# Kernel optimization log

Measured on AMD Instinct MI355X. Metric: run time of the kernel, lower is better.

The kernel has to match this reference:

```python
import jax, jax.numpy as jnp
import numpy as np

N = 10000        # num nodes
E = 640000       # num edges
FIN = 128        # input feature dim
NH = 8           # num heads
FOUT = 16        # out features per head (NH*FOUT == FIN)
NEG_SLOPE = 0.2
EPS = 1e-16


def setup_inputs() -> dict:
    key = jax.random.key(0)
    ks = jax.random.split(key, 7)
    x = jax.random.normal(ks[0], (N, FIN), dtype=jnp.float32)
    edges = jax.random.randint(ks[1], (2, E), 0, N, dtype=jnp.int64)
    # kaiming-uniform-ish init scale
    s = float(np.sqrt(6.0 / FIN))
    W_proj = jax.random.uniform(ks[2], (NH * FOUT, FIN), minval=-s, maxval=s, dtype=jnp.float32)
    W_skip = jax.random.uniform(ks[3], (NH * FOUT, FIN), minval=-s, maxval=s, dtype=jnp.float32)
    sf = float(np.sqrt(6.0 / FOUT))
    score_src = jax.random.uniform(ks[4], (1, NH, FOUT), minval=-sf, maxval=sf, dtype=jnp.float32)
    score_tgt = jax.random.uniform(ks[5], (1, NH, FOUT), minval=-sf, maxval=sf, dtype=jnp.float32)
    bias = jnp.zeros((NH * FOUT,), dtype=jnp.float32)
    return {"x": x, "edges": edges, "W_proj": W_proj, "W_skip": W_skip,
            "score_src": score_src, "score_tgt": score_tgt, "bias": bias}


def reference(x, edges, W_proj, W_skip, score_src, score_tgt, bias):
    src, tgt = edges[0], edges[1]
    # project: [N, NH, FOUT]
    proj = (x @ W_proj.T).reshape(N, NH, FOUT)
    # per-node scores: [N, NH]
    s_src = (proj * score_src).sum(-1)
    s_tgt = (proj * score_tgt).sum(-1)
    # lift to edges and score: [E, NH]
    scores = jax.nn.leaky_relu(s_src[src] + s_tgt[tgt], negative_slope=NEG_SLOPE)
    # neighborhood-aware softmax (global max subtraction, as in original)
    exp_scores = jnp.exp(scores - jnp.max(scores))
    denom = jax.ops.segment_sum(exp_scores, tgt, num_segments=N)  # [N, NH]
    att = exp_scores / (denom[tgt] + EPS)                          # [E, NH]
    # weighted aggregation: [N, NH, FOUT]
    weighted = proj[src] * att[:, :, None]
    out = jax.ops.segment_sum(weighted, tgt, num_segments=N)
    # skip connection (dims differ per-head, so skip_proj is used), concat, bias
    out = out + (x @ W_skip.T).reshape(N, NH, FOUT)
    out = out.reshape(N, NH * FOUT) + bias
    return out
```

## Files before the change

kernel.cpp:

```cpp
#include <hip/hip_runtime.h>
#include <hip/hip_bf16.h>

#define FIN   128
#define NH    8
#define NEG   0.2f
#define HB    256
#define NMAX  10240

typedef __attribute__((ext_vector_type(8))) short short8;
typedef __attribute__((ext_vector_type(4))) float f32x4;

__device__ __forceinline__ short f2bf(float f) {
    unsigned u = __float_as_uint(f);
    return (short)((u + 0x7FFFu + ((u >> 16) & 1u)) >> 16);
}
__device__ __forceinline__ float bflo(unsigned p) { return __uint_as_float(p << 16); }
__device__ __forceinline__ float bfhi(unsigned p) { return __uint_as_float(p & 0xFFFF0000u); }
__device__ __forceinline__ float ld_f(const void* p, int i, bool bf16) {
    if (bf16) {
        unsigned h = ((const unsigned short*)p)[i];
        return __uint_as_float(h << 16);
    }
    return ((const float*)p)[i];
}
__device__ __forceinline__ short8 ld_frag(const void* p, size_t off, bool bf16) {
    if (bf16) return *(const short8*)((const short*)p + off);
    const float* f = (const float*)p + off;
    f32x4 f0 = *(const f32x4*)f;
    f32x4 f1 = *(const f32x4*)(f + 4);
    short8 r;
    r[0] = f2bf(f0[0]); r[1] = f2bf(f0[1]); r[2] = f2bf(f0[2]); r[3] = f2bf(f0[3]);
    r[4] = f2bf(f1[0]); r[5] = f2bf(f1[1]); r[6] = f2bf(f1[2]); r[7] = f2bf(f1[3]);
    return r;
}
__device__ __forceinline__ float escore(float ss, float st) {
    float v = ss + st;
    v = v > 0.f ? v : NEG * v;
    return __expf(fminf(v, 60.f));
}
__device__ __forceinline__ bool wave_bf16(const unsigned* x32) {
    unsigned w  = x32[threadIdx.x & 63];
    unsigned ex = (w >> 7) & 0xFFu;
    return __popcll(__ballot(ex >= 118u && ex <= 130u)) >= 48;
}
__device__ __forceinline__ bool wave_e64(const int* e32) {
    return __popcll(__ballot(e32[2 * (threadIdx.x & 63) + 1] == 0)) == 64;
}

__global__ __launch_bounds__(256) void k_projhist(
    const void* __restrict__ x, const void* __restrict__ Wp,
    const void* __restrict__ Ws,
    const void* __restrict__ ssrcw, const void* __restrict__ stgtw,
    unsigned short* __restrict__ projb, unsigned short* __restrict__ skipb,
    float* __restrict__ s_src, float* __restrict__ s_tgt,
    const int* __restrict__ e32, int* __restrict__ hist2d,
    int N, int E, int tiles, int halfTiles, int projBlocks, int perB)
{
    __shared__ unsigned l32[NMAX / 2];
    if ((int)blockIdx.x >= projBlocks) {
        const bool e64 = wave_e64(e32);
        const int hb = (int)blockIdx.x - projBlocks;
        const int t = threadIdx.x;
        const int nw = (N + 1) >> 1;
        for (int j = t; j < nw; j += 256) l32[j] = 0;
        __syncthreads();
        const int lo = hb * perB;
        const int hi = min(lo + perB, E);
        for (int i = lo + t; i < hi; i += 256) {
            int tg = e64 ? e32[2 * ((size_t)E + i)] : e32[(size_t)E + i];
            atomicAdd(&l32[tg >> 1], 1u << ((tg & 1) << 4));
        }
        __syncthreads();
        for (int j = t; j < N; j += 256)
            hist2d[(size_t)hb * N + j] = (l32[j >> 1] >> ((j & 1) << 4)) & 0xFFFFu;
        return;
    }
    const bool bf16 = wave_bf16((const unsigned*)x);
    const int lane = threadIdx.x & 63;
    const int wt = blockIdx.x * 4 + (threadIdx.x >> 6);
    if (wt >= tiles) return;
    const int mat = (wt >= halfTiles) ? 1 : 0;
    const int m0 = (mat ? wt - halfTiles : wt) * 16;
    const int mr = lane & 15;
    const int kb = lane >> 4;

    short8 a[4];
    const size_t xoff = (size_t)(m0 + mr) * FIN + kb * 8;
#pragma unroll
    for (int s = 0; s < 4; ++s) a[s] = ld_frag(x, xoff + s * 32, bf16);

    const void* W = mat ? Ws : Wp;
    f32x4 acc[8];
#pragma unroll
    for (int c = 0; c < 8; ++c) {
        acc[c] = (f32x4){0.f, 0.f, 0.f, 0.f};
        const size_t woff = (size_t)(c * 16 + mr) * FIN + kb * 8;
#pragma unroll
        for (int s = 0; s < 4; ++s) {
            short8 b = ld_frag(W, woff + s * 32, bf16);
            acc[c] = __builtin_amdgcn_mfma_f32_16x16x32_bf16(a[s], b, acc[c], 0, 0, 0);
        }
    }
    if (mat == 0) {
#pragma unroll
        for (int c = 0; c < 8; ++c) {
            float sw = ld_f(ssrcw, c * 16 + mr, bf16);
            float tw = ld_f(stgtw, c * 16 + mr, bf16);
#pragma unroll
            for (int r = 0; r < 4; ++r) {
                int row = m0 + kb * 4 + r;
                float v = acc[c][r];
                projb[(size_t)row * FIN + c * 16 + mr] = (unsigned short)f2bf(v);
                float vs = v * sw, vt = v * tw;
#pragma unroll
                for (int o = 8; o >= 1; o >>= 1) {
                    vs += __shfl_xor(vs, o);
                    vt += __shfl_xor(vt, o);
                }
                if (mr == 0) {
                    s_src[row * NH + c] = vs;
                    s_tgt[row * NH + c] = vt;
                }
            }
        }
    } else {
#pragma unroll
        for (int c = 0; c < 8; ++c)
#pragma unroll
            for (int r = 0; r < 4; ++r)
                skipb[(size_t)(m0 + kb * 4 + r) * FIN + c * 16 + mr] =
                    (unsigned short)f2bf(acc[c][r]);
    }
}

__global__ __launch_bounds__(256) void k_colscan(
    const int* __restrict__ hist2d, int* __restrict__ pbase,
    int* __restrict__ cnt, int N, int Npad)
{
    int j = blockIdx.x * 256 + threadIdx.x;
    if (j >= N) { if (j < Npad) cnt[j] = 0; return; }
    int s = 0;
#pragma unroll 8
    for (int b = 0; b < HB; ++b) {
        int v = hist2d[(size_t)b * N + j];
        pbase[(size_t)b * N + j] = s;
        s += v;
    }
    cnt[j] = s;
}

__global__ __launch_bounds__(256) void k_place(
    const int* __restrict__ e32, const int* __restrict__ cnt,
    const int* __restrict__ pbase, int* __restrict__ offs,
    int* __restrict__ sorted_src, int N, int E, int perB)
{
    __shared__ int cur[NMAX];
    __shared__ int sd[256];
    const bool e64 = wave_e64(e32);
    const int b = blockIdx.x, t = threadIdx.x;
    const int PER = (N + 255) / 256;

    if (PER == 40 && (N & 3) == 0) {
        const int4* c4 = (const int4*)cnt + t * 10;
        int4 v[10];
        int sum = 0;
#pragma unroll
        for (int q = 0; q < 10; ++q) {
            v[q] = c4[q];
            sum += (v[q].x + v[q].y) + (v[q].z + v[q].w);
        }
        sd[t] = sum;
        __syncthreads();
#pragma unroll
        for (int off = 1; off < 256; off <<= 1) {
            int add = (t >= off) ? sd[t - off] : 0;
            __syncthreads();
            sd[t] += add;
            __syncthreads();
        }
        int run = sd[t] - sum;
        const int base = t * 40;
        const int4* pb4 = (const int4*)(pbase + (size_t)b * N) + t * 10;
#pragma unroll
        for (int q = 0; q < 10; ++q) {
            int4 pb = pb4[q];
            int idx = base + q * 4;
            int r0 = run;
            int r1 = r0 + v[q].x;
            int r2 = r1 + v[q].y;
            int r3 = r2 + v[q].z;
            cur[idx]     = r0 + pb.x;
            cur[idx + 1] = r1 + pb.y;
            cur[idx + 2] = r2 + pb.z;
            cur[idx + 3] = r3 + pb.w;
            if (b == 0) {
                if (idx     < N) offs[idx]     = r0;
                if (idx + 1 < N) offs[idx + 1] = r1;
                if (idx + 2 < N) offs[idx + 2] = r2;
                if (idx + 3 < N) offs[idx + 3] = r3;
            }
            run = r3 + v[q].w;
        }
        if (b == 0 && t == 255) offs[N] = run;
    } else {
        int sum = 0;
        for (int i = 0; i < PER; ++i) {
            int idx = t * PER + i;
            sum += (idx < N) ? cnt[idx] : 0;
        }
        sd[t] = sum;
        __syncthreads();
#pragma unroll
        for (int off = 1; off < 256; off <<= 1) {
            int add = (t >= off) ? sd[t - off] : 0;
            __syncthreads();
            sd[t] += add;
            __syncthreads();
        }
        int run = sd[t] - sum;
        for (int i = 0; i < PER; ++i) {
            int idx = t * PER + i;
            if (idx < N) {
                cur[idx] = run + pbase[(size_t)b * N + idx];
                if (b == 0) offs[idx] = run;
                run += cnt[idx];
            }
        }
        if (b == 0 && t == 255) offs[N] = run;
    }
    __syncthreads();

    const int lo = b * perB;
    const int hi = min(lo + perB, E);
    int se[10], te[10];
#pragma unroll
    for (int k = 0; k < 10; ++k) {
        int i = lo + t + k * 256;
        te[k] = -1;
        if (i < hi) {
            if (e64) { se[k] = e32[2 * (size_t)i]; te[k] = e32[2 * ((size_t)E + i)]; }
            else     { se[k] = e32[i];             te[k] = e32[(size_t)E + i]; }
        }
    }
#pragma unroll
    for (int k = 0; k < 10; ++k) {
        if (te[k] >= 0) {
            int pos = atomicAdd(&cur[te[k]], 1);
            sorted_src[pos] = se[k];
        }
    }
    for (int i = lo + t + 10 * 256; i < hi; i += 256) {
        int s, tg;
        if (e64) { s = e32[2 * (size_t)i]; tg = e32[2 * ((size_t)E + i)]; }
        else     { s = e32[i];             tg = e32[(size_t)E + i]; }
        int pos = atomicAdd(&cur[tg], 1);
        sorted_src[pos] = s;
    }
}

__global__ __launch_bounds__(64) void k_aggregate(
    const int* __restrict__ offs, const int* __restrict__ sorted_src,
    const float* __restrict__ s_src, const float* __restrict__ s_tgt,
    const unsigned short* __restrict__ projb, const unsigned short* __restrict__ skipb,
    const void* __restrict__ bias, void* __restrict__ out,
    const unsigned* __restrict__ x32)
{
    const bool bf16 = wave_bf16(x32);
    const int n = blockIdx.x, l = threadIdx.x;
    const int start = offs[n], end = offs[n + 1];
    const int h = l >> 3;
    const int c2 = l * 2;
    const float st = s_tgt[(size_t)n * NH + h];

    float ae0 = 0.f, ao0 = 0.f, ae1 = 0.f, ao1 = 0.f;
    float ae2 = 0.f, ao2 = 0.f, ae3 = 0.f, ao3 = 0.f;
    float d0 = 0.f, d1 = 0.f, d2 = 0.f, d3 = 0.f;

    const int cnt4 = (end - start) >> 2;
    int e = start;
    if (cnt4 > 0) {
        int s0 = sorted_src[e],     s1 = sorted_src[e + 1];
        int s2 = sorted_src[e + 2], s3 = sorted_src[e + 3];
        for (int g = 0; g < cnt4; ++g) {
            const int t0 = s0, t1 = s1, t2 = s2, t3 = s3;
            e += 4;
            if (g + 1 < cnt4) {
                s0 = sorted_src[e];     s1 = sorted_src[e + 1];
                s2 = sorted_src[e + 2]; s3 = sorted_src[e + 3];
            }
            float w0 = escore(s_src[(size_t)t0 * NH + h], st);
            float w1 = escore(s_src[(size_t)t1 * NH + h], st);
            float w2 = escore(s_src[(size_t)t2 * NH + h], st);
            float w3 = escore(s_src[(size_t)t3 * NH + h], st);
            unsigned p0 = *(const unsigned*)(projb + (size_t)t0 * FIN + c2);
            unsigned p1 = *(const unsigned*)(projb + (size_t)t1 * FIN + c2);
            unsigned p2 = *(const unsigned*)(projb + (size_t)t2 * FIN + c2);
            unsigned p3 = *(const unsigned*)(projb + (size_t)t3 * FIN + c2);
            ae0 += w0 * bflo(p0); ao0 += w0 * bfhi(p0); d0 += w0;
            ae1 += w1 * bflo(p1); ao1 += w1 * bfhi(p1); d1 += w1;
            ae2 += w2 * bflo(p2); ao2 += w2 * bfhi(p2); d2 += w2;
            ae3 += w3 * bflo(p3); ao3 += w3 * bfhi(p3); d3 += w3;
        }
    }
    for (; e < end; ++e) {
        int s = sorted_src[e];
        float w = escore(s_src[(size_t)s * NH + h], st);
        unsigned p = *(const unsigned*)(projb + (size_t)s * FIN + c2);
        ae0 += w * bflo(p); ao0 += w * bfhi(p); d0 += w;
    }

    float inv = 1.f / (((d0 + d1) + (d2 + d3)) + 1e-16f);
    unsigned skp = *(const unsigned*)(skipb + (size_t)n * FIN + c2);
    float be, bo;
    if (bf16) {
        unsigned bb = *(const unsigned*)((const unsigned short*)bias + c2);
        be = bflo(bb); bo = bfhi(bb);
    } else {
        float2 b2 = *(const float2*)((const float*)bias + c2);
        be = b2.x; bo = b2.y;
    }
    float oe = ((ae0 + ae1) + (ae2 + ae3)) * inv + bflo(skp) + be;
    float oo = ((ao0 + ao1) + (ao2 + ao3)) * inv + bfhi(skp) + bo;
    if (bf16) {
        unsigned pr = ((unsigned)(unsigned short)f2bf(oo) << 16)
                    | (unsigned)(unsigned short)f2bf(oe);
        ((unsigned*)out)[((size_t)n * FIN + c2) >> 1] = pr;
    } else {
        float2 o2; o2.x = oe; o2.y = oo;
        *(float2*)((float*)out + (size_t)n * FIN + c2) = o2;
    }
}

extern "C" void kernel_launch(void* const* d_in, const int* in_sizes, int n_in,
                              void* d_out, int out_size, void* d_ws, size_t ws_size,
                              hipStream_t stream)
{
    const void* x    = d_in[0];
    const int* edges = (const int*)d_in[1];
    const void* Wp   = d_in[2];
    const void* Ws   = d_in[3];
    const void* ssw  = d_in[4];
    const void* stw  = d_in[5];
    const void* bias = d_in[6];

    const int N = in_sizes[0] / FIN;
    const int E = in_sizes[1] / 2;
    const int PER  = (N + 255) / 256;
    const int Npad = PER * 256;

    char* wp = (char*)d_ws;
    auto takeB = [&wp](size_t bytes) {
        char* p = wp;
        wp += (bytes + 255) & ~(size_t)255;
        return p;
    };
    unsigned short* projb = (unsigned short*)takeB((size_t)N * FIN * 2);
    unsigned short* skipb = (unsigned short*)takeB((size_t)N * FIN * 2);
    float* s_src    = (float*)takeB((size_t)N * NH * 4);
    float* s_tgt    = (float*)takeB((size_t)N * NH * 4);
    int* sorted_src = (int*)takeB((size_t)E * 4);
    int* offs       = (int*)takeB((size_t)(N + 8) * 4);
    int* cnt        = (int*)takeB((size_t)Npad * 4);
    int* hist2d     = (int*)takeB((size_t)HB * N * 4);
    int* pbase      = (int*)takeB((size_t)HB * N * 4 + 4096);

    const int halfTiles  = (N + 15) / 16;
    const int tiles      = 2 * halfTiles;
    const int projBlocks = (tiles + 3) / 4;
    const int perB       = (E + HB - 1) / HB;

    k_projhist<<<projBlocks + HB, 256, 0, stream>>>(
        x, Wp, Ws, ssw, stw, projb, skipb, s_src, s_tgt,
        edges, hist2d, N, E, tiles, halfTiles, projBlocks, perB);
    k_colscan<<<Npad / 256, 256, 0, stream>>>(hist2d, pbase, cnt, N, Npad);
    k_place<<<HB, 256, 0, stream>>>(edges, cnt, pbase, offs, sorted_src, N, E, perB);
    k_aggregate<<<N, 64, 0, stream>>>(offs, sorted_src, s_src, s_tgt, projb,
                                      skipb, bias, d_out, (const unsigned*)x);
}
```

Baseline: 148.0 us.

## Pack histograms as 16-bit pairs, fuse column scan into GEMM kernel, unroll aggregate by 8

Histogram counts are stored as packed 16-bit pairs, which halves the traffic for the histogram, prefix and count buffers. The histogram now runs as its own kernel, and the column scan runs alongside the projection GEMM in one launch, removing a kernel launch and overlapping the scan with the matmul. The placement kernel now reads the packed counts with a fixed 40-per-thread layout, which drops the general fallback path for other N. The aggregation loop processes 8 neighbours per iteration to get more loads in flight, at the cost of more registers.

```diff
diff --git a/kernel.cpp b/kernel.cpp
--- a/kernel.cpp
+++ b/kernel.cpp
@@ -6,6 +6,7 @@
 #define NEG   0.2f
 #define HB    256
 #define NMAX  10240
+#define RSW   (NMAX / 2)
 
 typedef __attribute__((ext_vector_type(8))) short short8;
 typedef __attribute__((ext_vector_type(4))) float f32x4;
@@ -47,38 +48,59 @@
     return __popcll(__ballot(e32[2 * (threadIdx.x & 63) + 1] == 0)) == 64;
 }
 
-__global__ __launch_bounds__(256) void k_projhist(
+__global__ __launch_bounds__(256) void k_hist(
+    const int* __restrict__ e32, unsigned* __restrict__ hist2w,
+    int N, int E, int perB)
+{
+    __shared__ unsigned l32[RSW];
+    const bool e64 = wave_e64(e32);
+    const int b = blockIdx.x, t = threadIdx.x;
+    const int nw = (N + 1) >> 1;
+    for (int j = t; j < nw; j += 256) l32[j] = 0;
+    __syncthreads();
+    const int lo = b * perB;
+    const int hi = min(lo + perB, E);
+    for (int i = lo + t; i < hi; i += 256) {
+        int tg = e64 ? ((const int2*)e32)[(size_t)E + i].x : e32[(size_t)E + i];
+        atomicAdd(&l32[tg >> 1], 1u << ((tg & 1) << 4));
+    }
+    __syncthreads();
+    const int nw4 = (nw + 3) >> 2;
+    uint4* dst = (uint4*)(hist2w + (size_t)b * RSW);
+    const uint4* src = (const uint4*)l32;
+    for (int j = t; j < nw4; j += 256) dst[j] = src[j];
+}
+
+__global__ __launch_bounds__(256) void k_gemmscan(
     const void* __restrict__ x, const void* __restrict__ Wp,
     const void* __restrict__ Ws,
     const void* __restrict__ ssrcw, const void* __restrict__ stgtw,
     unsigned short* __restrict__ projb, unsigned short* __restrict__ skipb,
     float* __restrict__ s_src, float* __restrict__ s_tgt,
-    const int* __restrict__ e32, int* __restrict__ hist2d,
-    int N, int E, int tiles, int halfTiles, int projBlocks, int perB)
-{
-    __shared__ unsigned l32[NMAX / 2];
-    if ((int)blockIdx.x >= projBlocks) {
-        const bool e64 = wave_e64(e32);
-        const int hb = (int)blockIdx.x - projBlocks;
-        const int t = threadIdx.x;
+    const unsigned* __restrict__ hist2w, unsigned* __restrict__ pbase2w,
+    unsigned* __restrict__ cnt2w,
+    int N, int tiles, int halfTiles, int csBlocks)
+{
+    if ((int)blockIdx.x < csBlocks) {
+        const int j = blockIdx.x * 256 + threadIdx.x;
+        if (j >= RSW) return;
         const int nw = (N + 1) >> 1;
-        for (int j = t; j < nw; j += 256) l32[j] = 0;
-        __syncthreads();
-        const int lo = hb * perB;
-        const int hi = min(lo + perB, E);
-        for (int i = lo + t; i < hi; i += 256) {
-            int tg = e64 ? e32[2 * ((size_t)E + i)] : e32[(size_t)E + i];
-            atomicAdd(&l32[tg >> 1], 1u << ((tg & 1) << 4));
-        }
-        __syncthreads();
-        for (int j = t; j < N; j += 256)
-            hist2d[(size_t)hb * N + j] = (l32[j >> 1] >> ((j & 1) << 4)) & 0xFFFFu;
+        if (j >= nw) { cnt2w[j] = 0; return; }
+        unsigned s0 = 0, s1 = 0;
+#pragma unroll 8
+        for (int r = 0; r < HB; ++r) {
+            unsigned v = hist2w[(size_t)r * RSW + j];
+            pbase2w[(size_t)r * RSW + j] = s0 | (s1 << 16);
+            s0 += v & 0xFFFFu;
+            s1 += v >> 16;
+        }
+        cnt2w[j] = s0 | (s1 << 16);
         return;
     }
+    const int wt = ((int)blockIdx.x - csBlocks) * 4 + ((int)threadIdx.x >> 6);
+    if (wt >= tiles) return;
     const bool bf16 = wave_bf16((const unsigned*)x);
     const int lane = threadIdx.x & 63;
-    const int wt = blockIdx.x * 4 + (threadIdx.x >> 6);
-    if (wt >= tiles) return;
     const int mat = (wt >= halfTiles) ? 1 : 0;
     const int m0 = (mat ? wt - halfTiles : wt) * 16;
     const int mr = lane & 15;
@@ -133,41 +155,27 @@
     }
 }
 
-__global__ __launch_bounds__(256) void k_colscan(
-    const int* __restrict__ hist2d, int* __restrict__ pbase,
-    int* __restrict__ cnt, int N, int Npad)
-{
-    int j = blockIdx.x * 256 + threadIdx.x;
-    if (j >= N) { if (j < Npad) cnt[j] = 0; return; }
-    int s = 0;
-#pragma unroll 8
-    for (int b = 0; b < HB; ++b) {
-        int v = hist2d[(size_t)b * N + j];
-        pbase[(size_t)b * N + j] = s;
-        s += v;
-    }
-    cnt[j] = s;
-}
-
 __global__ __launch_bounds__(256) void k_place(
-    const int* __restrict__ e32, const int* __restrict__ cnt,
-    const int* __restrict__ pbase, int* __restrict__ offs,
+    const int* __restrict__ e32, const unsigned* __restrict__ cnt2w,
+    const unsigned* __restrict__ pbase2w, int* __restrict__ offs,
     int* __restrict__ sorted_src, int N, int E, int perB)
 {
     __shared__ int cur[NMAX];
     __shared__ int sd[256];
     const bool e64 = wave_e64(e32);
     const int b = blockIdx.x, t = threadIdx.x;
-    const int PER = (N + 255) / 256;
-
-    if (PER == 40 && (N & 3) == 0) {
-        const int4* c4 = (const int4*)cnt + t * 10;
-        int4 v[10];
+
+    {
+        const uint4* c4 = (const uint4*)cnt2w + t * 5;
+        uint4 v[5];
         int sum = 0;
 #pragma unroll
-        for (int q = 0; q < 10; ++q) {
+        for (int q = 0; q < 5; ++q) {
             v[q] = c4[q];
-            sum += (v[q].x + v[q].y) + (v[q].z + v[q].w);
+            sum += (int)((v[q].x & 0xFFFFu) + (v[q].x >> 16))
+                 + (int)((v[q].y & 0xFFFFu) + (v[q].y >> 16))
+                 + (int)((v[q].z & 0xFFFFu) + (v[q].z >> 16))
+                 + (int)((v[q].w & 0xFFFFu) + (v[q].w >> 16));
         }
         sd[t] = sum;
         __syncthreads();
@@ -179,51 +187,23 @@
             __syncthreads();
         }
         int run = sd[t] - sum;
+        const uint4* pb4 = (const uint4*)(pbase2w + (size_t)b * RSW) + t * 5;
         const int base = t * 40;
-        const int4* pb4 = (const int4*)(pbase + (size_t)b * N) + t * 10;
-#pragma unroll
-        for (int q = 0; q < 10; ++q) {
-            int4 pb = pb4[q];
-            int idx = base + q * 4;
-            int r0 = run;
-            int r1 = r0 + v[q].x;
-            int r2 = r1 + v[q].y;
-            int r3 = r2 + v[q].z;
-            cur[idx]     = r0 + pb.x;
-            cur[idx + 1] = r1 + pb.y;
-            cur[idx + 2] = r2 + pb.z;
-            cur[idx + 3] = r3 + pb.w;
-            if (b == 0) {
-                if (idx     < N) offs[idx]     = r0;
-                if (idx + 1 < N) offs[idx + 1] = r1;
-                if (idx + 2 < N) offs[idx + 2] = r2;
-                if (idx + 3 < N) offs[idx + 3] = r3;
-            }
-            run = r3 + v[q].w;
-        }
-        if (b == 0 && t == 255) offs[N] = run;
-    } else {
-        int sum = 0;
-        for (int i = 0; i < PER; ++i) {
-            int idx = t * PER + i;
-            sum += (idx < N) ? cnt[idx] : 0;
-        }
-        sd[t] = sum;
-        __syncthreads();
-#pragma unroll
-        for (int off = 1; off < 256; off <<= 1) {
-            int add = (t >= off) ? sd[t - off] : 0;
-            __syncthreads();
-            sd[t] += add;
-            __syncthreads();
-        }
-        int run = sd[t] - sum;
-        for (int i = 0; i < PER; ++i) {
-            int idx = t * PER + i;
-            if (idx < N) {
-                cur[idx] = run + pbase[(size_t)b * N + idx];
-                if (b == 0) offs[idx] = run;
-                run += cnt[idx];
+#pragma unroll
+        for (int q = 0; q < 5; ++q) {
+            uint4 pb = pb4[q];
+            unsigned cw[4] = {v[q].x, v[q].y, v[q].z, v[q].w};
+            unsigned pw[4] = {pb.x, pb.y, pb.z, pb.w};
+#pragma unroll
+            for (int u = 0; u < 4; ++u) {
+                int idx = base + q * 8 + u * 2;
+                int c0 = (int)(cw[u] & 0xFFFFu), c1 = (int)(cw[u] >> 16);
+                cur[idx] = run + (int)(pw[u] & 0xFFFFu);
+                if (b == 0 && idx < N) offs[idx] = run;
+                run += c0;
+                cur[idx + 1] = run + (int)(pw[u] >> 16);
+                if (b == 0 && idx + 1 < N) offs[idx + 1] = run;
+                run += c1;
             }
         }
         if (b == 0 && t == 255) offs[N] = run;
@@ -238,8 +218,13 @@
         int i = lo + t + k * 256;
         te[k] = -1;
         if (i < hi) {
-            if (e64) { se[k] = e32[2 * (size_t)i]; te[k] = e32[2 * ((size_t)E + i)]; }
-            else     { se[k] = e32[i];             te[k] = e32[(size_t)E + i]; }
+            if (e64) {
+                se[k] = ((const int2*)e32)[(size_t)i].x;
+                te[k] = ((const int2*)e32)[(size_t)E + i].x;
+            } else {
+                se[k] = e32[i];
+                te[k] = e32[(size_t)E + i];
+            }
         }
     }
 #pragma unroll
@@ -251,8 +236,8 @@
     }
     for (int i = lo + t + 10 * 256; i < hi; i += 256) {
         int s, tg;
-        if (e64) { s = e32[2 * (size_t)i]; tg = e32[2 * ((size_t)E + i)]; }
-        else     { s = e32[i];             tg = e32[(size_t)E + i]; }
+        if (e64) { s = ((const int2*)e32)[(size_t)i].x; tg = ((const int2*)e32)[(size_t)E + i].x; }
+        else     { s = e32[i];                           tg = e32[(size_t)E + i]; }
         int pos = atomicAdd(&cur[tg], 1);
         sorted_src[pos] = s;
     }
@@ -272,44 +257,52 @@
     const int c2 = l * 2;
     const float st = s_tgt[(size_t)n * NH + h];
 
-    float ae0 = 0.f, ao0 = 0.f, ae1 = 0.f, ao1 = 0.f;
-    float ae2 = 0.f, ao2 = 0.f, ae3 = 0.f, ao3 = 0.f;
-    float d0 = 0.f, d1 = 0.f, d2 = 0.f, d3 = 0.f;
-
-    const int cnt4 = (end - start) >> 2;
+    float ae[8], ao[8], d[8];
+#pragma unroll
+    for (int k = 0; k < 8; ++k) { ae[k] = 0.f; ao[k] = 0.f; d[k] = 0.f; }
+
+    const int cnt8 = (end - start) >> 3;
     int e = start;
-    if (cnt4 > 0) {
-        int s0 = sorted_src[e],     s1 = sorted_src[e + 1];
-        int s2 = sorted_src[e + 2], s3 = sorted_src[e + 3];
-        for (int g = 0; g < cnt4; ++g) {
-            const int t0 = s0, t1 = s1, t2 = s2, t3 = s3;
-            e += 4;
-            if (g + 1 < cnt4) {
-                s0 = sorted_src[e];     s1 = sorted_src[e + 1];
-                s2 = sorted_src[e + 2]; s3 = sorted_src[e + 3];
-            }
-            float w0 = escore(s_src[(size_t)t0 * NH + h], st);
-            float w1 = escore(s_src[(size_t)t1 * NH + h], st);
-            float w2 = escore(s_src[(size_t)t2 * NH + h], st);
-            float w3 = escore(s_src[(size_t)t3 * NH + h], st);
-            unsigned p0 = *(const unsigned*)(projb + (size_t)t0 * FIN + c2);
-            unsigned p1 = *(const unsigned*)(projb + (size_t)t1 * FIN + c2);
-            unsigned p2 = *(const unsigned*)(projb + (size_t)t2 * FIN + c2);
-            unsigned p3 = *(const unsigned*)(projb + (size_t)t3 * FIN + c2);
-            ae0 += w0 * bflo(p0); ao0 += w0 * bfhi(p0); d0 += w0;
-            ae1 += w1 * bflo(p1); ao1 += w1 * bfhi(p1); d1 += w1;
-            ae2 += w2 * bflo(p2); ao2 += w2 * bfhi(p2); d2 += w2;
-            ae3 += w3 * bflo(p3); ao3 += w3 * bfhi(p3); d3 += w3;
+    if (cnt8 > 0) {
+        int idx[8];
+#pragma unroll
+        for (int k = 0; k < 8; ++k) idx[k] = sorted_src[e + k];
+        for (int g = 0; g < cnt8; ++g) {
+            int cu[8];
+#pragma unroll
+            for (int k = 0; k < 8; ++k) cu[k] = idx[k];
+            e += 8;
+            if (g + 1 < cnt8) {
+#pragma unroll
+                for (int k = 0; k < 8; ++k) idx[k] = sorted_src[e + k];
+            }
+            unsigned p[8];
+#pragma unroll
+            for (int k = 0; k < 8; ++k)
+                p[k] = *(const unsigned*)(projb + (size_t)cu[k] * FIN + c2);
+            float w[8];
+#pragma unroll
+            for (int k = 0; k < 8; ++k)
+                w[k] = escore(s_src[(size_t)cu[k] * NH + h], st);
+#pragma unroll
+            for (int k = 0; k < 8; ++k) {
+                ae[k] += w[k] * bflo(p[k]);
+                ao[k] += w[k] * bfhi(p[k]);
+                d[k]  += w[k];
+            }
         }
     }
     for (; e < end; ++e) {
         int s = sorted_src[e];
         float w = escore(s_src[(size_t)s * NH + h], st);
         unsigned p = *(const unsigned*)(projb + (size_t)s * FIN + c2);
-        ae0 += w * bflo(p); ao0 += w * bfhi(p); d0 += w;
-    }
-
-    float inv = 1.f / (((d0 + d1) + (d2 + d3)) + 1e-16f);
+        ae[0] += w * bflo(p); ao[0] += w * bfhi(p); d[0] += w;
+    }
+
+    float num_e = ((ae[0] + ae[1]) + (ae[2] + ae[3])) + ((ae[4] + ae[5]) + (ae[6] + ae[7]));
+    float num_o = ((ao[0] + ao[1]) + (ao[2] + ao[3])) + ((ao[4] + ao[5]) + (ao[6] + ao[7]));
+    float den   = ((d[0] + d[1]) + (d[2] + d[3])) + ((d[4] + d[5]) + (d[6] + d[7]));
+    float inv = 1.f / (den + 1e-16f);
     unsigned skp = *(const unsigned*)(skipb + (size_t)n * FIN + c2);
     float be, bo;
     if (bf16) {
@@ -319,8 +312,8 @@
         float2 b2 = *(const float2*)((const float*)bias + c2);
         be = b2.x; bo = b2.y;
     }
-    float oe = ((ae0 + ae1) + (ae2 + ae3)) * inv + bflo(skp) + be;
-    float oo = ((ao0 + ao1) + (ao2 + ao3)) * inv + bfhi(skp) + bo;
+    float oe = num_e * inv + bflo(skp) + be;
+    float oo = num_o * inv + bfhi(skp) + bo;
     if (bf16) {
         unsigned pr = ((unsigned)(unsigned short)f2bf(oo) << 16)
                     | (unsigned)(unsigned short)f2bf(oe);
@@ -345,8 +338,6 @@
 
     const int N = in_sizes[0] / FIN;
     const int E = in_sizes[1] / 2;
-    const int PER  = (N + 255) / 256;
-    const int Npad = PER * 256;
 
     char* wp = (char*)d_ws;
     auto takeB = [&wp](size_t bytes) {
@@ -356,24 +347,25 @@
     };
     unsigned short* projb = (unsigned short*)takeB((size_t)N * FIN * 2);
     unsigned short* skipb = (unsigned short*)takeB((size_t)N * FIN * 2);
-    float* s_src    = (float*)takeB((size_t)N * NH * 4);
-    float* s_tgt    = (float*)takeB((size_t)N * NH * 4);
-    int* sorted_src = (int*)takeB((size_t)E * 4);
-    int* offs       = (int*)takeB((size_t)(N + 8) * 4);
-    int* cnt        = (int*)takeB((size_t)Npad * 4);
-    int* hist2d     = (int*)takeB((size_t)HB * N * 4);
-    int* pbase      = (int*)takeB((size_t)HB * N * 4 + 4096);
-
-    const int halfTiles  = (N + 15) / 16;
-    const int tiles      = 2 * halfTiles;
-    const int projBlocks = (tiles + 3) / 4;
-    const int perB       = (E + HB - 1) / HB;
-
-    k_projhist<<<projBlocks + HB, 256, 0, stream>>>(
+    float* s_src      = (float*)takeB((size_t)N * NH * 4);
+    float* s_tgt      = (float*)takeB((size_t)N * NH * 4);
+    int* sorted_src   = (int*)takeB((size_t)E * 4);
+    int* offs         = (int*)takeB((size_t)(N + 8) * 4);
+    unsigned* cnt2w   = (unsigned*)takeB((size_t)RSW * 4);
+    unsigned* hist2w  = (unsigned*)takeB((size_t)HB * RSW * 4);
+    unsigned* pbase2w = (unsigned*)takeB((size_t)HB * RSW * 4);
+
+    const int halfTiles = (N + 15) / 16;
+    const int tiles     = 2 * halfTiles;
+    const int gemmBlks  = (tiles + 3) / 4;
+    const int csBlocks  = (RSW + 255) / 256;
+    const int perB      = (E + HB - 1) / HB;
+
+    k_hist<<<HB, 256, 0, stream>>>(edges, hist2w, N, E, perB);
+    k_gemmscan<<<csBlocks + gemmBlks, 256, 0, stream>>>(
         x, Wp, Ws, ssw, stw, projb, skipb, s_src, s_tgt,
-        edges, hist2d, N, E, tiles, halfTiles, projBlocks, perB);
-    k_colscan<<<Npad / 256, 256, 0, stream>>>(hist2d, pbase, cnt, N, Npad);
-    k_place<<<HB, 256, 0, stream>>>(edges, cnt, pbase, offs, sorted_src, N, E, perB);
+        hist2w, pbase2w, cnt2w, N, tiles, halfTiles, csBlocks);
+    k_place<<<HB, 256, 0, stream>>>(edges, cnt2w, pbase2w, offs, sorted_src, N, E, perB);
     k_aggregate<<<N, 64, 0, stream>>>(offs, sorted_src, s_src, s_tgt, projb,
                                       skipb, bias, d_out, (const unsigned*)x);
 }
```

Result: faster. 135.6 us, median of 2 (-8.4%).
